# Optimization experiments

Hardware: AMD Instinct MI355X
Metric: run time of the kernel (lower is better)

## Reference

```python
import jax, jax.numpy as jnp
import numpy as np

D_FEAT = 8192   # feature-space dimension d
T_RES = 2048    # number of reservoir feature vectors
P_PARAMS = 16   # n_modes * ansatz_layers
ORDER = 16      # agp_krylov_order (Krylov/Lanczos subspace size)
DTAU = 0.08     # cfg.ite_dtau
REG = 1e-4      # cfg.agp_reg
EPS = 1e-15


def setup_inputs() -> dict:
    key = jax.random.key(0)
    k1, k2, k3 = jax.random.split(key, 3)
    f = jax.random.normal(k1, (D_FEAT,), jnp.float32)
    # scale so spectral radius of H = -R^T R times DTAU is O(1)
    R = jax.random.normal(k2, (T_RES, D_FEAT), jnp.float32) * 0.02
    D = jax.random.normal(k3, (P_PARAMS, D_FEAT), jnp.float32)
    return {"f": f, "R": R, "D": D}


def _forward(f, R, D):
    d = f.shape[0]
    l = ORDER

    def apply_H(v):
        # H v = -sum_t f_t (f_t . v)  == -R^T (R v), matrix-free, memory-bound
        return -jnp.einsum('td,t->d', R, jnp.einsum('td,d->t', R, v))

    # ITE residual F = -(H - E) f, E = <f, Hf> / <f, f>
    Hf = apply_H(f)
    E = jnp.dot(f, Hf) / (jnp.dot(f, f) + EPS)
    F = -(Hf - E * f)
    normF = jnp.linalg.norm(F)

    # Lanczos with full reorthogonalisation; Q has l+1 rows (last is scratch)
    Q0 = jnp.zeros((l + 1, d), f.dtype).at[0].set(F / normF)
    alpha0 = jnp.zeros((l,), f.dtype)
    beta0 = jnp.zeros((l,), f.dtype)

    def step(carry, j):
        Q, alpha, beta = carry
        qj = Q[j]
        w = apply_H(qj)
        a = jnp.dot(qj, w)
        alpha = alpha.at[j].set(a)
        w = w - a * qj
        jm1 = jnp.maximum(j - 1, 0)
        bprev = jnp.where(j > 0, beta[jm1], jnp.array(0.0, f.dtype))
        w = w - bprev * Q[jm1]
        # full reorthogonalisation; rows > j of Q are zero so this projects
        # exactly onto span{q_0..q_j} like the original k-loop
        w = w - jnp.einsum('kd,k->d', Q, jnp.einsum('kd,d->k', Q, w))
        b = jnp.linalg.norm(w)
        beta = beta.at[j].set(b)
        Q = Q.at[j + 1].set(w / jnp.maximum(b, 1e-30))
        return (Q, alpha, beta), None

    (Q, alpha, beta), _ = jax.lax.scan(step, (Q0, alpha0, beta0), jnp.arange(l))
    Qb = Q[:l]          # (l, d) orthonormal Krylov basis
    off = beta[:l - 1]  # off-diagonal of tridiagonal T

    # Krylov exponential: exp(-H dtau) F ~= ||F|| * Q^T expm(-T dtau) e0
    Tmat = jnp.diag(alpha) + jnp.diag(off, 1) + jnp.diag(off, -1)
    evals, V = jnp.linalg.eigh(Tmat)
    coeffs = normF * (V @ (jnp.exp(-evals * DTAU) * V[0]))
    direction = jnp.einsum('l,ld->d', coeffs, Qb)

    # per-parameter diagonal projection: dtheta_i = <df_i, dir>/(||df_i||^2 + reg)
    dtheta = (D @ direction) / (jnp.sum(D * D, axis=1) + REG)
    return dtheta


def reference(f, R, D):
    return _forward(f, R, D)
```

## Files before the change

kernel.cpp:

```cpp
#include <hip/hip_runtime.h>
#include <math.h>

#define D_FEAT 8192
#define NC4    2048
#define T_RES  2048
#define LORD   16

#define NTHR 512
#define NBLK 256
#define RPT  32
#define NOWN 32
#define CH   64
#define NREPA 4
#define NREPB 16

#define G_COEF  0
#define G_FUPA  16
#define G_FREDB (G_FUPA + 17*NREPA*256)
#define G_FCOEF (G_FREDB + 17*NREPB*16)
#define G_FNUM  (G_FCOEF + NREPB*16)
#define G_ZEND  (G_FNUM + NREPA*256)
#define G_URAW  G_ZEND
#define G_UUP   (G_URAW + 17*2048)
#define G_FFP   (G_UUP + 32)
#define G_B2P   (G_FFP + 256)
#define G_DP    (G_B2P + 16*256)
#define G_NUMP  (G_DP + 16*16*32)
#define G_DENP  (G_NUMP + 16*256)
#define G_UPB   ((G_DENP + 16*256 + 1023) & ~1023)
#define UPSLOT  (NOWN*NBLK*CH)

__device__ __forceinline__ void astore(float* p, float v) {
    __hip_atomic_store(p, v, __ATOMIC_RELAXED, __HIP_MEMORY_SCOPE_AGENT);
}
__device__ __forceinline__ void astoreu(unsigned* p, unsigned v) {
    __hip_atomic_store(p, v, __ATOMIC_RELAXED, __HIP_MEMORY_SCOPE_AGENT);
}
__device__ __forceinline__ unsigned aloadu(const unsigned* p) {
    return __hip_atomic_load(p, __ATOMIC_RELAXED, __HIP_MEMORY_SCOPE_AGENT);
}

__device__ __forceinline__ void sigA(unsigned* fl, int bid) {
    __syncthreads();
    if (threadIdx.x < NREPA) astoreu(&fl[threadIdx.x*256 + bid], 1u);
}
__device__ __forceinline__ void pollA(const unsigned* fl, int bid) {
    if (threadIdx.x < 64) {
        const unsigned* p = fl + (bid & (NREPA-1))*256 + 4*threadIdx.x;
        for (;;) {
            unsigned a = aloadu(p) & aloadu(p+1) & aloadu(p+2) & aloadu(p+3);
            if (__all((int)a)) break;
            __builtin_amdgcn_s_sleep(2);
        }
    }
    __syncthreads();
}

__device__ __forceinline__ void sigB(unsigned* fl, int bid) {
    __syncthreads();
    if (threadIdx.x < NREPB)
        __hip_atomic_fetch_or(&fl[threadIdx.x*16], 1u << bid,
                              __ATOMIC_RELAXED, __HIP_MEMORY_SCOPE_AGENT);
}
__device__ __forceinline__ void pollB(const unsigned* fl, int bid) {
    if (threadIdx.x == 0)
        while (aloadu(&fl[(bid & (NREPB-1))*16]) != 0xFFFFFFFFu)
            __builtin_amdgcn_s_sleep(2);
    __syncthreads();
}

__device__ __forceinline__ float wave_sum64(float s) {
    #pragma unroll
    for (int m = 1; m < 64; m <<= 1) s += __shfl_xor(s, m, 64);
    return s;
}
__device__ __forceinline__ float sum32(float s) {
    #pragma unroll
    for (int m = 1; m < 32; m <<= 1) s += __shfl_xor(s, m, 64);
    return s;
}

__device__ __forceinline__ void u_pass_lds(const float4 (&rr)[RPT],
                                           const float* wsl, float* ubuf,
                                           int rg, int cg) {
    const float4 w4 = ((const float4*)wsl)[cg];
    #pragma unroll
    for (int i = 0; i < RPT; ++i) {
        float d = rr[i].x*w4.x + rr[i].y*w4.y + rr[i].z*w4.z + rr[i].w*w4.w;
        d += __shfl_xor(d, 1, 64);
        d += __shfl_xor(d, 2, 64);
        d += __shfl_xor(d, 4, 64);
        if (cg == 0) ubuf[rg + 64*i] = d;
    }
}

__device__ __forceinline__ void flush_up(float* UP, const float* ubuf,
                                         int bid, int tid) {
    #pragma unroll
    for (int r = 0; r < 4; ++r) {
        const int t = tid + 512*r;
        astore(&UP[(size_t)(t >> 6)*(NBLK*CH) + bid*CH + (t & 63)], ubuf[t]);
    }
}

__device__ __forceinline__ void reduce_up64(const float* __restrict__ UP,
                                            float* udst, float (*red8)[CH],
                                            float* ufin64, float* uhrow,
                                            int bid, int tid) {
    const int r = tid & 63, bg = tid >> 6;
    const float* base = UP + (size_t)bid*(NBLK*CH);
    float s = 0.f;
    #pragma unroll
    for (int m = 0; m < 32; ++m) s += base[(bg*32 + m)*CH + r];
    red8[bg][r] = s;
    __syncthreads();
    if (tid < 64) {
        float u = 0.f;
        #pragma unroll
        for (int g = 0; g < 8; ++g) u += red8[g][tid];
        ufin64[tid] = u;
        uhrow[tid] = u;
        astore(&udst[bid*CH + tid], u);
    }
    __syncthreads();
}

__device__ __forceinline__ float4 y_pass(const float4 (&rr)[RPT],
                                         const float* u, int rg) {
    float4 acc = make_float4(0.f, 0.f, 0.f, 0.f);
    #pragma unroll
    for (int i = 0; i < RPT; ++i) {
        const float ut = u[rg + 64*i];
        acc.x -= ut*rr[i].x; acc.y -= ut*rr[i].y;
        acc.z -= ut*rr[i].z; acc.w -= ut*rr[i].w;
    }
    return acc;
}

__device__ __forceinline__ void y_reduce(float4 acc, float (*red)[8][4],
                                         float* ysl, int wave, int lane, int tid) {
    #pragma unroll
    for (int m = 8; m < 64; m <<= 1) {
        acc.x += __shfl_xor(acc.x, m, 64); acc.y += __shfl_xor(acc.y, m, 64);
        acc.z += __shfl_xor(acc.z, m, 64); acc.w += __shfl_xor(acc.w, m, 64);
    }
    if (lane < 8) {
        red[wave][lane][0] = acc.x; red[wave][lane][1] = acc.y;
        red[wave][lane][2] = acc.z; red[wave][lane][3] = acc.w;
    }
    __syncthreads();
    if (tid < 32) {
        const int g = tid >> 2, comp = tid & 3;
        float s = 0.f;
        #pragma unroll
        for (int w = 0; w < 8; ++w) s += red[w][g][comp];
        ysl[g*4 + comp] = s;
    }
    __syncthreads();
}

__global__ __launch_bounds__(NTHR, 2) void k_all(
    const float* __restrict__ Rm, const float* __restrict__ f,
    const float* __restrict__ Dm, float* __restrict__ out,
    float* __restrict__ ws)
{
    __shared__ __align__(16) float ubuf[2048];
    __shared__ float red8[8][CH];
    __shared__ float red[8][8][4];
    __shared__ float ufin64[CH];
    __shared__ float uh[17][CH];
    __shared__ __align__(16) float ysl[32];
    __shared__ __align__(16) float dirs[32];
    __shared__ __align__(16) float fsl[32];
    __shared__ float Wh[LORD][32];
    __shared__ float bh[LORD];
    __shared__ float alph[LORD];
    __shared__ float dotl[LORD];
    __shared__ float cf[LORD];
    __shared__ float misc[4];

    float* coefg    = ws + G_COEF;
    unsigned* fupA  = (unsigned*)(ws + G_FUPA);
    unsigned* fredB = (unsigned*)(ws + G_FREDB);
    unsigned* fcoef = (unsigned*)(ws + G_FCOEF);
    unsigned* fnum  = (unsigned*)(ws + G_FNUM);
    float* uraw = ws + G_URAW;
    float* UUP  = ws + G_UUP;
    float* FFP  = ws + G_FFP;
    float* B2P  = ws + G_B2P;
    float* DP   = ws + G_DP;
    float* NUMP = ws + G_NUMP;
    float* DENP = ws + G_DENP;
    float* UPB  = ws + G_UPB;

    const int tid = threadIdx.x, bid = blockIdx.x;
    const int cg = tid & 7, rg = tid >> 3;
    const int lane = tid & 63, wave = tid >> 6;
    const bool owner = bid < NOWN;

    const float4* R4 = (const float4*)Rm;
    float4 rr[RPT];
    #pragma unroll
    for (int i = 0; i < RPT; ++i)
        rr[i] = R4[(size_t)(rg + 64*i)*NC4 + (bid << 3) + cg];

    if (wave == 0) {
        float4 fv = make_float4(0.f, 0.f, 0.f, 0.f);
        if (lane < 8) { fv = ((const float4*)f)[(bid << 3) + lane];
                        ((float4*)fsl)[lane] = fv; }
        float s2 = fv.x*fv.x + fv.y*fv.y + fv.z*fv.z + fv.w*fv.w;
        s2 += __shfl_xor(s2, 1, 64);
        s2 += __shfl_xor(s2, 2, 64);
        s2 += __shfl_xor(s2, 4, 64);
        if (lane == 0) astore(&FFP[bid], s2);
    }
    __syncthreads();
    u_pass_lds(rr, fsl, ubuf, rg, cg);
    __syncthreads();
    flush_up(UPB + (size_t)16*UPSLOT, ubuf, bid, tid);
    sigA(fupA + 16*NREPA*256, bid);

    if (owner) {
        pollA(fupA + 16*NREPA*256, bid);
        reduce_up64(UPB + (size_t)16*UPSLOT, uraw + 16*2048, red8, ufin64,
                    uh[16], bid, tid);
        if (wave == 0) {
            float p = ufin64[lane]*ufin64[lane];
            p = wave_sum64(p);
            if (lane == 0) astore(&UUP[bid], p);
        }
        sigB(fredB + 16*NREPB*16, bid);
    }
    pollB(fredB + 16*NREPB*16, bid);

    if (wave == 0) {
        float s = (lane < NOWN) ? UUP[lane] : 0.f;
        s = sum32(s);
        if (lane == 0) misc[3] = s;
    }
    if (wave == 1) {
        float s = 0.f;
        #pragma unroll
        for (int i = 0; i < 4; ++i) s += FFP[lane + 64*i];
        s = wave_sum64(s);
        if (lane == 0) misc[2] = s;
    }
    #pragma unroll
    for (int r = 0; r < 4; ++r)
        ubuf[tid + 512*r] = uraw[16*2048 + tid + 512*r];
    __syncthreads();
    {
        float4 acc = y_pass(rr, ubuf, rg);
        y_reduce(acc, red, ysl, wave, lane, tid);
        const float E = -misc[3] / (misc[2] + 1e-15f);
        float v = 0.f;
        if (tid < 32) { v = E*fsl[tid] - ysl[tid]; Wh[0][tid] = v; }
        if (wave == 0) {
            float s = (lane < 32) ? v*v : 0.f;
            s = wave_sum64(s);
            if (lane == 0) astore(&B2P[0*256 + bid], s);
        }
        __syncthreads();
        u_pass_lds(rr, Wh[0], ubuf, rg, cg);
        __syncthreads();
        flush_up(UPB + (size_t)0*UPSLOT, ubuf, bid, tid);
    }
    sigA(fupA + 0*NREPA*256, bid);

    for (int j = 0; j < LORD; ++j) {
        float* UPj = UPB + (size_t)j*UPSLOT;
        float* DPj = DP + j*(16*NOWN);
        if (owner) {
            pollA(fupA + j*NREPA*256, bid);
            reduce_up64(UPj, uraw + (size_t)j*2048, red8, ufin64, uh[j],
                        bid, tid);
            for (int k = wave; k <= j; k += 8) {
                float p = ufin64[lane] * uh[k][lane];
                p = wave_sum64(p);
                if (lane == 0) astore(&DPj[k*NOWN + bid], p);
            }
            sigB(fredB + j*NREPB*16, bid);
        }
        pollB(fredB + j*NREPB*16, bid);

        float tmp[4];
        if (j < LORD - 1) {
            #pragma unroll
            for (int r = 0; r < 4; ++r)
                tmp[r] = uraw[(size_t)j*2048 + tid + 512*r];
        }
        for (int k = wave; k <= j; k += 8) {
            float s = (lane < NOWN) ? DPj[k*NOWN + lane] : 0.f;
            s = sum32(s);
            if (lane == 0) dotl[k] = s;
        }
        if (wave == 1) {
            float s = 0.f;
            #pragma unroll
            for (int i = 0; i < 4; ++i) s += B2P[j*256 + lane + 64*i];
            s = wave_sum64(s);
            if (lane == 0) misc[0] = s;
        }
        __syncthreads();
        const float b2j = misc[0];
        const float bj  = sqrtf(fmaxf(b2j, 1e-60f));
        if (tid == 0) {
            bh[j]   = bj;
            alph[j] = -dotl[j] / fmaxf(b2j, 1e-60f);
        }
        if (j < LORD - 1) {
            const float inv = 1.0f / bj;
            #pragma unroll
            for (int r = 0; r < 4; ++r) ubuf[tid + 512*r] = tmp[r] * inv;
            __syncthreads();
            float4 acc = y_pass(rr, ubuf, rg);
            y_reduce(acc, red, ysl, wave, lane, tid);
            float v = 0.f;
            if (tid < 32) {
                v = ysl[tid];
                for (int k = 0; k <= j; ++k)
                    v += (dotl[k] / (bj * bh[k] * bh[k])) * Wh[k][tid];
                Wh[j+1][tid] = v;
            }
            if (wave == 0) {
                float s = (lane < 32) ? v*v : 0.f;
                s = wave_sum64(s);
                if (lane == 0) astore(&B2P[(j+1)*256 + bid], s);
            }
            __syncthreads();
            u_pass_lds(rr, Wh[j+1], ubuf, rg, cg);
            __syncthreads();
            flush_up(UPB + (size_t)(j+1)*UPSLOT, ubuf, bid, tid);
            sigA(fupA + (j+1)*NREPA*256, bid);
        } else {
            __syncthreads();
            if (bid == 0 && wave == 0) {
                double a = 0.0, bl = 0.0;
                if (lane < LORD)     a  = (double)alph[lane];
                if (lane < LORD - 1) bl = (double)bh[lane + 1];
                double bprev = __shfl_up(bl, 1, 64);
                if (lane == 0) bprev = 0.0;
                if (lane >= LORD) { a = 0.0; bl = 0.0; bprev = 0.0; }
                double v = (lane == 0) ? 1.0 : 0.0;
                double accd = v;
                for (int n = 1; n <= 30; ++n) {
                    double vm = __shfl_up(v, 1, 64);
                    if (lane == 0) vm = 0.0;
                    double vp = __shfl_down(v, 1, 64);
                    if (lane >= LORD - 1) vp = 0.0;
                    const double tv = a*v + bprev*vm + bl*vp;
                    v = tv * (-0.08 / (double)n);
                    accd += v;
                }
                if (lane < LORD)
                    astore(&coefg[lane], (float)accd * bh[0]);
            }
            __syncthreads();
            if (bid == 0 && tid < NREPB) astoreu(&fcoef[tid*16], 1u);
            if (tid == 0)
                while (aloadu(&fcoef[(bid & (NREPB-1))*16]) == 0u)
                    __builtin_amdgcn_s_sleep(2);
            __syncthreads();
        }
    }

    if (wave == 0 && lane < 16) cf[lane] = coefg[lane];
    __syncthreads();
    if (tid < 32) {
        float s = 0.f;
        #pragma unroll
        for (int l = 0; l < LORD; ++l) s += cf[l] * Wh[l][tid] / bh[l];
        dirs[tid] = s;
    }
    __syncthreads();
    if (wave == 0 && lane < 16) {
        const float4* Dp = (const float4*)Dm + (size_t)lane*NC4 + (bid << 3);
        float num = 0.f, den = 0.f;
        #pragma unroll
        for (int g = 0; g < 8; ++g) {
            const float4 dv = Dp[g];
            const float4 dr = ((const float4*)dirs)[g];
            num += dv.x*dr.x + dv.y*dr.y + dv.z*dr.z + dv.w*dr.w;
            den += dv.x*dv.x + dv.y*dv.y + dv.z*dv.z + dv.w*dv.w;
        }
        astore(&NUMP[lane*256 + bid], num);
        astore(&DENP[lane*256 + bid], den);
    }
    sigA(fnum, bid);

    if (bid == 0) {
        pollA(fnum, 0);
        for (int p = wave; p < 16; p += 8) {
            float n = 0.f, d = 0.f;
            #pragma unroll
            for (int i = 0; i < 4; ++i) {
                n += NUMP[p*256 + lane + 64*i];
                d += DENP[p*256 + lane + 64*i];
            }
            n = wave_sum64(n);
            d = wave_sum64(d);
            if (lane == 0) out[p] = n / (d + 1e-4f);
        }
    }
}

extern "C" void kernel_launch(void* const* d_in, const int* in_sizes, int n_in,
                              void* d_out, int out_size, void* d_ws, size_t ws_size,
                              hipStream_t stream)
{
    (void)in_sizes; (void)n_in; (void)out_size; (void)ws_size;
    const float* f  = (const float*)d_in[0];
    const float* Rm = (const float*)d_in[1];
    const float* Dm = (const float*)d_in[2];
    float* outp = (float*)d_out;
    float* ws   = (float*)d_ws;
    hipMemsetAsync(ws, 0, G_ZEND * sizeof(float), stream);
    void* args[] = { (void*)&Rm, (void*)&f, (void*)&Dm, (void*)&outp, (void*)&ws };
    hipLaunchCooperativeKernel((const void*)k_all, dim3(NBLK), dim3(NTHR),
                               args, 0, stream);
}
```

Baseline: 314.1 us.

## Remap register tile to whole rows per thread and widen owner reduction

Each thread now holds 4 full R rows across the block's 32 columns instead of 32 rows by 4 columns. The u-pass dot products therefore finish in registers without shuffles or an LDS staging buffer, and partials are written with 64-bit atomic stores. The cross-block u reduction is split over 64 owner blocks of 32 rows each, which needs a 64-bit bitmask barrier and a new butterfly-style y reduction. The 1/beta scaling moves after the y reduction. This trades LDS traffic and syncs for more shuffle work in the y pass and more owner participation.

New measurement: 535.2 us. +70.4%, slower.

```diff
diff --git a/kernel.cpp b/kernel.cpp
--- a/kernel.cpp
+++ b/kernel.cpp
@@ -8,11 +8,11 @@
 
 #define NTHR 512
 #define NBLK 256
-#define RPT  32
-#define NOWN 32
-#define CH   64
-#define NREPA 4
+#define CH   32
+#define NOWN 64
+#define NREPA 8
 #define NREPB 16
+#define UPSLOT (NBLK*T_RES)
 
 #define G_COEF  0
 #define G_FUPA  16
@@ -22,21 +22,26 @@
 #define G_ZEND  (G_FNUM + NREPA*256)
 #define G_URAW  G_ZEND
 #define G_UUP   (G_URAW + 17*2048)
-#define G_FFP   (G_UUP + 32)
+#define G_FFP   (G_UUP + 64)
 #define G_B2P   (G_FFP + 256)
 #define G_DP    (G_B2P + 16*256)
-#define G_NUMP  (G_DP + 16*16*32)
+#define G_NUMP  (G_DP + 16*16*64)
 #define G_DENP  (G_NUMP + 16*256)
 #define G_UPB   ((G_DENP + 16*256 + 1023) & ~1023)
-#define UPSLOT  (NOWN*NBLK*CH)
 
 __device__ __forceinline__ void astore(float* p, float v) {
     __hip_atomic_store(p, v, __ATOMIC_RELAXED, __HIP_MEMORY_SCOPE_AGENT);
 }
+__device__ __forceinline__ void astore64(unsigned long long* p, unsigned long long v) {
+    __hip_atomic_store(p, v, __ATOMIC_RELAXED, __HIP_MEMORY_SCOPE_AGENT);
+}
 __device__ __forceinline__ void astoreu(unsigned* p, unsigned v) {
     __hip_atomic_store(p, v, __ATOMIC_RELAXED, __HIP_MEMORY_SCOPE_AGENT);
 }
 __device__ __forceinline__ unsigned aloadu(const unsigned* p) {
+    return __hip_atomic_load(p, __ATOMIC_RELAXED, __HIP_MEMORY_SCOPE_AGENT);
+}
+__device__ __forceinline__ unsigned long long aload64(const unsigned long long* p) {
     return __hip_atomic_load(p, __ATOMIC_RELAXED, __HIP_MEMORY_SCOPE_AGENT);
 }
 
@@ -59,12 +64,14 @@
 __device__ __forceinline__ void sigB(unsigned* fl, int bid) {
     __syncthreads();
     if (threadIdx.x < NREPB)
-        __hip_atomic_fetch_or(&fl[threadIdx.x*16], 1u << bid,
-                              __ATOMIC_RELAXED, __HIP_MEMORY_SCOPE_AGENT);
+        __hip_atomic_fetch_or((unsigned long long*)(fl + threadIdx.x*16),
+                              1ULL << bid, __ATOMIC_RELAXED,
+                              __HIP_MEMORY_SCOPE_AGENT);
 }
 __device__ __forceinline__ void pollB(const unsigned* fl, int bid) {
     if (threadIdx.x == 0)
-        while (aloadu(&fl[(bid & (NREPB-1))*16]) != 0xFFFFFFFFu)
+        while (aload64((const unsigned long long*)(fl + (bid & (NREPB-1))*16))
+               != 0xFFFFFFFFFFFFFFFFULL)
             __builtin_amdgcn_s_sleep(2);
     __syncthreads();
 }
@@ -80,73 +87,86 @@
     return s;
 }
 
-__device__ __forceinline__ void u_pass_lds(const float4 (&rr)[RPT],
-                                           const float* wsl, float* ubuf,
-                                           int rg, int cg) {
-    const float4 w4 = ((const float4*)wsl)[cg];
+__device__ __forceinline__ float4 f4add(float4 a, float4 b) {
+    return make_float4(a.x+b.x, a.y+b.y, a.z+b.z, a.w+b.w);
+}
+__device__ __forceinline__ float4 f4shfl_xor(float4 v, int m) {
+    float4 r;
+    r.x = __shfl_xor(v.x, m, 64); r.y = __shfl_xor(v.y, m, 64);
+    r.z = __shfl_xor(v.z, m, 64); r.w = __shfl_xor(v.w, m, 64);
+    return r;
+}
+
+__device__ __forceinline__ void u_pass_row(const float4 (&rr)[4][8],
+                                           const float* wsl, float (&out)[4]) {
+    float4 w4[8];
     #pragma unroll
-    for (int i = 0; i < RPT; ++i) {
-        float d = rr[i].x*w4.x + rr[i].y*w4.y + rr[i].z*w4.z + rr[i].w*w4.w;
-        d += __shfl_xor(d, 1, 64);
-        d += __shfl_xor(d, 2, 64);
-        d += __shfl_xor(d, 4, 64);
-        if (cg == 0) ubuf[rg + 64*i] = d;
-    }
-}
-
-__device__ __forceinline__ void flush_up(float* UP, const float* ubuf,
-                                         int bid, int tid) {
+    for (int c = 0; c < 8; ++c) w4[c] = ((const float4*)wsl)[c];
     #pragma unroll
     for (int r = 0; r < 4; ++r) {
-        const int t = tid + 512*r;
-        astore(&UP[(size_t)(t >> 6)*(NBLK*CH) + bid*CH + (t & 63)], ubuf[t]);
-    }
-}
-
-__device__ __forceinline__ void reduce_up64(const float* __restrict__ UP,
-                                            float* udst, float (*red8)[CH],
-                                            float* ufin64, float* uhrow,
-                                            int bid, int tid) {
-    const int r = tid & 63, bg = tid >> 6;
-    const float* base = UP + (size_t)bid*(NBLK*CH);
-    float s = 0.f;
-    #pragma unroll
-    for (int m = 0; m < 32; ++m) s += base[(bg*32 + m)*CH + r];
-    red8[bg][r] = s;
-    __syncthreads();
-    if (tid < 64) {
-        float u = 0.f;
-        #pragma unroll
-        for (int g = 0; g < 8; ++g) u += red8[g][tid];
-        ufin64[tid] = u;
-        uhrow[tid] = u;
-        astore(&udst[bid*CH + tid], u);
-    }
-    __syncthreads();
-}
-
-__device__ __forceinline__ float4 y_pass(const float4 (&rr)[RPT],
-                                         const float* u, int rg) {
-    float4 acc = make_float4(0.f, 0.f, 0.f, 0.f);
-    #pragma unroll
-    for (int i = 0; i < RPT; ++i) {
-        const float ut = u[rg + 64*i];
-        acc.x -= ut*rr[i].x; acc.y -= ut*rr[i].y;
-        acc.z -= ut*rr[i].z; acc.w -= ut*rr[i].w;
-    }
-    return acc;
-}
-
-__device__ __forceinline__ void y_reduce(float4 acc, float (*red)[8][4],
-                                         float* ysl, int wave, int lane, int tid) {
-    #pragma unroll
-    for (int m = 8; m < 64; m <<= 1) {
-        acc.x += __shfl_xor(acc.x, m, 64); acc.y += __shfl_xor(acc.y, m, 64);
-        acc.z += __shfl_xor(acc.z, m, 64); acc.w += __shfl_xor(acc.w, m, 64);
-    }
+        float d0 = rr[r][0].x*w4[0].x + rr[r][0].y*w4[0].y + rr[r][0].z*w4[0].z + rr[r][0].w*w4[0].w;
+        float d1 = rr[r][1].x*w4[1].x + rr[r][1].y*w4[1].y + rr[r][1].z*w4[1].z + rr[r][1].w*w4[1].w;
+        float d2 = rr[r][2].x*w4[2].x + rr[r][2].y*w4[2].y + rr[r][2].z*w4[2].z + rr[r][2].w*w4[2].w;
+        float d3 = rr[r][3].x*w4[3].x + rr[r][3].y*w4[3].y + rr[r][3].z*w4[3].z + rr[r][3].w*w4[3].w;
+        float d4 = rr[r][4].x*w4[4].x + rr[r][4].y*w4[4].y + rr[r][4].z*w4[4].z + rr[r][4].w*w4[4].w;
+        float d5 = rr[r][5].x*w4[5].x + rr[r][5].y*w4[5].y + rr[r][5].z*w4[5].z + rr[r][5].w*w4[5].w;
+        float d6 = rr[r][6].x*w4[6].x + rr[r][6].y*w4[6].y + rr[r][6].z*w4[6].z + rr[r][6].w*w4[6].w;
+        float d7 = rr[r][7].x*w4[7].x + rr[r][7].y*w4[7].y + rr[r][7].z*w4[7].z + rr[r][7].w*w4[7].w;
+        out[r] = ((d0+d1)+(d2+d3)) + ((d4+d5)+(d6+d7));
+    }
+}
+
+__device__ __forceinline__ void flush4(float* UP, const float (&out)[4],
+                                       int h, int bid) {
+    const int t0 = h << 2;
+    float* dst = &UP[(size_t)(t0 >> 5)*(NBLK*CH) + bid*CH + (t0 & 31)];
+    unsigned long long p0, p1;
+    __builtin_memcpy(&p0, &out[0], 8);
+    __builtin_memcpy(&p1, &out[2], 8);
+    astore64((unsigned long long*)dst, p0);
+    astore64((unsigned long long*)(dst + 2), p1);
+}
+
+__device__ __forceinline__ void y_reduce8(const float4 (&acc)[8],
+                                          float (*red)[8][4], float* ysl,
+                                          int wave, int lane, int tid) {
+    const bool b0 = lane & 1, b1 = lane & 2, b2 = lane & 4;
+    float4 h0_0, h0_1, h0_2, h0_3;
+    {
+        float4 s0 = b0 ? acc[0] : acc[4];
+        float4 s1 = b0 ? acc[1] : acc[5];
+        float4 s2 = b0 ? acc[2] : acc[6];
+        float4 s3 = b0 ? acc[3] : acc[7];
+        float4 r0 = f4shfl_xor(s0, 1), r1 = f4shfl_xor(s1, 1);
+        float4 r2 = f4shfl_xor(s2, 1), r3 = f4shfl_xor(s3, 1);
+        h0_0 = f4add(b0 ? acc[4] : acc[0], r0);
+        h0_1 = f4add(b0 ? acc[5] : acc[1], r1);
+        h0_2 = f4add(b0 ? acc[6] : acc[2], r2);
+        h0_3 = f4add(b0 ? acc[7] : acc[3], r3);
+    }
+    float4 h1_0, h1_1;
+    {
+        float4 s0 = b1 ? h1_0 : h0_2;
+        (void)s0;
+        float4 t0 = b1 ? h0_0 : h0_2;
+        float4 t1 = b1 ? h0_1 : h0_3;
+        float4 r0 = f4shfl_xor(t0, 2), r1 = f4shfl_xor(t1, 2);
+        h1_0 = f4add(b1 ? h0_2 : h0_0, r0);
+        h1_1 = f4add(b1 ? h0_3 : h0_1, r1);
+    }
+    float4 h2;
+    {
+        float4 t0 = b2 ? h1_0 : h1_1;
+        float4 r0 = f4shfl_xor(t0, 4);
+        h2 = f4add(b2 ? h1_1 : h1_0, r0);
+    }
+    h2 = f4add(h2, f4shfl_xor(h2, 8));
+    h2 = f4add(h2, f4shfl_xor(h2, 16));
+    h2 = f4add(h2, f4shfl_xor(h2, 32));
     if (lane < 8) {
-        red[wave][lane][0] = acc.x; red[wave][lane][1] = acc.y;
-        red[wave][lane][2] = acc.z; red[wave][lane][3] = acc.w;
+        const int G = ((lane & 1) << 2) | (lane & 2) | ((lane >> 2) & 1);
+        red[wave][G][0] = h2.x; red[wave][G][1] = h2.y;
+        red[wave][G][2] = h2.z; red[wave][G][3] = h2.w;
     }
     __syncthreads();
     if (tid < 32) {
@@ -164,15 +184,14 @@
     const float* __restrict__ Dm, float* __restrict__ out,
     float* __restrict__ ws)
 {
-    __shared__ __align__(16) float ubuf[2048];
-    __shared__ float red8[8][CH];
     __shared__ float red[8][8][4];
-    __shared__ float ufin64[CH];
-    __shared__ float uh[17][CH];
+    __shared__ float red2[32][17];
+    __shared__ float ufin32[32];
+    __shared__ float uh[17][32];
     __shared__ __align__(16) float ysl[32];
     __shared__ __align__(16) float dirs[32];
     __shared__ __align__(16) float fsl[32];
-    __shared__ float Wh[LORD][32];
+    __shared__ __align__(16) float Wh[LORD][32];
     __shared__ float bh[LORD];
     __shared__ float alph[LORD];
     __shared__ float dotl[LORD];
@@ -194,15 +213,16 @@
     float* UPB  = ws + G_UPB;
 
     const int tid = threadIdx.x, bid = blockIdx.x;
-    const int cg = tid & 7, rg = tid >> 3;
     const int lane = tid & 63, wave = tid >> 6;
     const bool owner = bid < NOWN;
 
     const float4* R4 = (const float4*)Rm;
-    float4 rr[RPT];
+    float4 rr[4][8];
     #pragma unroll
-    for (int i = 0; i < RPT; ++i)
-        rr[i] = R4[(size_t)(rg + 64*i)*NC4 + (bid << 3) + cg];
+    for (int r = 0; r < 4; ++r)
+        #pragma unroll
+        for (int c = 0; c < 8; ++c)
+            rr[r][c] = R4[(size_t)((tid << 2) + r)*NC4 + (bid << 3) + c];
 
     if (wave == 0) {
         float4 fv = make_float4(0.f, 0.f, 0.f, 0.f);
@@ -215,27 +235,44 @@
         if (lane == 0) astore(&FFP[bid], s2);
     }
     __syncthreads();
-    u_pass_lds(rr, fsl, ubuf, rg, cg);
-    __syncthreads();
-    flush_up(UPB + (size_t)16*UPSLOT, ubuf, bid, tid);
+    {
+        float uo[4];
+        u_pass_row(rr, fsl, uo);
+        flush4(UPB + (size_t)16*UPSLOT, uo, tid, bid);
+    }
     sigA(fupA + 16*NREPA*256, bid);
 
     if (owner) {
         pollA(fupA + 16*NREPA*256, bid);
-        reduce_up64(UPB + (size_t)16*UPSLOT, uraw + 16*2048, red8, ufin64,
-                    uh[16], bid, tid);
+        const float* base = UPB + (size_t)16*UPSLOT + (size_t)bid*(NBLK*CH);
+        const int r = tid & 31, q = tid >> 5;
+        float s = 0.f;
+        #pragma unroll
+        for (int i = 0; i < 16; ++i) s += base[(q*16 + i)*CH + r];
+        red2[r][q] = s;
+        __syncthreads();
+        if (tid < 32) {
+            float u = 0.f;
+            #pragma unroll
+            for (int q2 = 0; q2 < 16; ++q2) u += red2[tid][q2];
+            ufin32[tid] = u;
+            uh[16][tid] = u;
+            astore(&uraw[16*2048 + bid*CH + tid], u);
+        }
+        __syncthreads();
         if (wave == 0) {
-            float p = ufin64[lane]*ufin64[lane];
-            p = wave_sum64(p);
+            float p = (lane < 32) ? ufin32[lane]*ufin32[lane] : 0.f;
+            p = sum32(p);
             if (lane == 0) astore(&UUP[bid], p);
         }
         sigB(fredB + 16*NREPB*16, bid);
     }
     pollB(fredB + 16*NREPB*16, bid);
 
+    float4 u4 = ((const float4*)(uraw + 16*2048))[tid];
     if (wave == 0) {
-        float s = (lane < NOWN) ? UUP[lane] : 0.f;
-        s = sum32(s);
+        float s = UUP[lane];
+        s = wave_sum64(s);
         if (lane == 0) misc[3] = s;
     }
     if (wave == 1) {
@@ -245,13 +282,21 @@
         s = wave_sum64(s);
         if (lane == 0) misc[2] = s;
     }
-    #pragma unroll
-    for (int r = 0; r < 4; ++r)
-        ubuf[tid + 512*r] = uraw[16*2048 + tid + 512*r];
-    __syncthreads();
     {
-        float4 acc = y_pass(rr, ubuf, rg);
-        y_reduce(acc, red, ysl, wave, lane, tid);
+        float4 acc[8];
+        #pragma unroll
+        for (int c = 0; c < 8; ++c) acc[c] = make_float4(0.f, 0.f, 0.f, 0.f);
+        const float ua[4] = {u4.x, u4.y, u4.z, u4.w};
+        #pragma unroll
+        for (int r = 0; r < 4; ++r) {
+            const float ut = ua[r];
+            #pragma unroll
+            for (int c = 0; c < 8; ++c) {
+                acc[c].x -= ut*rr[r][c].x; acc[c].y -= ut*rr[r][c].y;
+                acc[c].z -= ut*rr[r][c].z; acc[c].w -= ut*rr[r][c].w;
+            }
+        }
+        y_reduce8(acc, red, ysl, wave, lane, tid);
         const float E = -misc[3] / (misc[2] + 1e-15f);
         float v = 0.f;
         if (tid < 32) { v = E*fsl[tid] - ysl[tid]; Wh[0][tid] = v; }
@@ -261,9 +306,9 @@
             if (lane == 0) astore(&B2P[0*256 + bid], s);
         }
         __syncthreads();
-        u_pass_lds(rr, Wh[0], ubuf, rg, cg);
-        __syncthreads();
-        flush_up(UPB + (size_t)0*UPSLOT, ubuf, bid, tid);
+        float uo[4];
+        u_pass_row(rr, Wh[0], uo);
+        flush4(UPB + (size_t)0*UPSLOT, uo, tid, bid);
     }
     sigA(fupA + 0*NREPA*256, bid);
 
@@ -272,26 +317,37 @@
         float* DPj = DP + j*(16*NOWN);
         if (owner) {
             pollA(fupA + j*NREPA*256, bid);
-            reduce_up64(UPj, uraw + (size_t)j*2048, red8, ufin64, uh[j],
-                        bid, tid);
+            const float* base = UPj + (size_t)bid*(NBLK*CH);
+            const int r = tid & 31, q = tid >> 5;
+            float s = 0.f;
+            #pragma unroll
+            for (int i = 0; i < 16; ++i) s += base[(q*16 + i)*CH + r];
+            red2[r][q] = s;
+            __syncthreads();
+            if (tid < 32) {
+                float u = 0.f;
+                #pragma unroll
+                for (int q2 = 0; q2 < 16; ++q2) u += red2[tid][q2];
+                ufin32[tid] = u;
+                uh[j][tid] = u;
+                astore(&uraw[(size_t)j*2048 + bid*CH + tid], u);
+            }
+            __syncthreads();
             for (int k = wave; k <= j; k += 8) {
-                float p = ufin64[lane] * uh[k][lane];
-                p = wave_sum64(p);
+                float p = (lane < 32) ? ufin32[lane]*uh[k][lane] : 0.f;
+                p = sum32(p);
                 if (lane == 0) astore(&DPj[k*NOWN + bid], p);
             }
             sigB(fredB + j*NREPB*16, bid);
         }
         pollB(fredB + j*NREPB*16, bid);
 
-        float tmp[4];
-        if (j < LORD - 1) {
-            #pragma unroll
-            for (int r = 0; r < 4; ++r)
-                tmp[r] = uraw[(size_t)j*2048 + tid + 512*r];
-        }
+        float4 uj4 = make_float4(0.f, 0.f, 0.f, 0.f);
+        if (j < LORD - 1)
+            uj4 = ((const float4*)(uraw + (size_t)j*2048))[tid];
         for (int k = wave; k <= j; k += 8) {
-            float s = (lane < NOWN) ? DPj[k*NOWN + lane] : 0.f;
-            s = sum32(s);
+            float s = DPj[k*NOWN + lane];
+            s = wave_sum64(s);
             if (lane == 0) dotl[k] = s;
         }
         if (wave == 1) {
@@ -309,15 +365,24 @@
             alph[j] = -dotl[j] / fmaxf(b2j, 1e-60f);
         }
         if (j < LORD - 1) {
+            float4 acc[8];
+            #pragma unroll
+            for (int c = 0; c < 8; ++c) acc[c] = make_float4(0.f, 0.f, 0.f, 0.f);
+            const float ua[4] = {uj4.x, uj4.y, uj4.z, uj4.w};
+            #pragma unroll
+            for (int r = 0; r < 4; ++r) {
+                const float ut = ua[r];
+                #pragma unroll
+                for (int c = 0; c < 8; ++c) {
+                    acc[c].x -= ut*rr[r][c].x; acc[c].y -= ut*rr[r][c].y;
+                    acc[c].z -= ut*rr[r][c].z; acc[c].w -= ut*rr[r][c].w;
+                }
+            }
+            y_reduce8(acc, red, ysl, wave, lane, tid);
             const float inv = 1.0f / bj;
-            #pragma unroll
-            for (int r = 0; r < 4; ++r) ubuf[tid + 512*r] = tmp[r] * inv;
-            __syncthreads();
-            float4 acc = y_pass(rr, ubuf, rg);
-            y_reduce(acc, red, ysl, wave, lane, tid);
             float v = 0.f;
             if (tid < 32) {
-                v = ysl[tid];
+                v = ysl[tid] * inv;
                 for (int k = 0; k <= j; ++k)
                     v += (dotl[k] / (bj * bh[k] * bh[k])) * Wh[k][tid];
                 Wh[j+1][tid] = v;
@@ -328,9 +393,9 @@
                 if (lane == 0) astore(&B2P[(j+1)*256 + bid], s);
             }
             __syncthreads();
-            u_pass_lds(rr, Wh[j+1], ubuf, rg, cg);
-            __syncthreads();
-            flush_up(UPB + (size_t)(j+1)*UPSLOT, ubuf, bid, tid);
+            float uo[4];
+            u_pass_row(rr, Wh[j+1], uo);
+            flush4(UPB + (size_t)(j+1)*UPSLOT, uo, tid, bid);
             sigA(fupA + (j+1)*NREPA*256, bid);
         } else {
             __syncthreads();
```

## Double owner blocks for the reduction and compute Krylov coefficients redundantly per block

Applied to the files above, without the earlier changes.

Raises the number of reducer (owner) blocks from 32 to 64, each reducing a 32-wide chunk instead of 64, which halves the serial reduction work per owner. The phase-B flag changes from a single bitmask fetch_or to per-owner flags polled by a wave. Every block now computes the final Taylor-series coefficients itself, which removes a grid-wide broadcast and wait through global memory. The cost is more flag traffic and polling, plus redundant double-precision work in every block.

Result: faster. 307.2 us (-2.2%).

```diff
diff --git a/kernel.cpp b/kernel.cpp
--- a/kernel.cpp
+++ b/kernel.cpp
@@ -9,23 +9,21 @@
 #define NTHR 512
 #define NBLK 256
 #define RPT  32
-#define NOWN 32
-#define CH   64
-#define NREPA 4
+#define NOWN 64
+#define CH   32
+#define NREPA 8
 #define NREPB 16
 
-#define G_COEF  0
-#define G_FUPA  16
+#define G_FUPA  0
 #define G_FREDB (G_FUPA + 17*NREPA*256)
-#define G_FCOEF (G_FREDB + 17*NREPB*16)
-#define G_FNUM  (G_FCOEF + NREPB*16)
+#define G_FNUM  (G_FREDB + 17*NREPB*NOWN)
 #define G_ZEND  (G_FNUM + NREPA*256)
 #define G_URAW  G_ZEND
 #define G_UUP   (G_URAW + 17*2048)
-#define G_FFP   (G_UUP + 32)
+#define G_FFP   (G_UUP + 64)
 #define G_B2P   (G_FFP + 256)
 #define G_DP    (G_B2P + 16*256)
-#define G_NUMP  (G_DP + 16*16*32)
+#define G_NUMP  (G_DP + 16*16*64)
 #define G_DENP  (G_NUMP + 16*256)
 #define G_UPB   ((G_DENP + 16*256 + 1023) & ~1023)
 #define UPSLOT  (NOWN*NBLK*CH)
@@ -58,14 +56,14 @@
 
 __device__ __forceinline__ void sigB(unsigned* fl, int bid) {
     __syncthreads();
-    if (threadIdx.x < NREPB)
-        __hip_atomic_fetch_or(&fl[threadIdx.x*16], 1u << bid,
-                              __ATOMIC_RELAXED, __HIP_MEMORY_SCOPE_AGENT);
+    if (threadIdx.x < NREPB) astoreu(&fl[threadIdx.x*NOWN + bid], 1u);
 }
 __device__ __forceinline__ void pollB(const unsigned* fl, int bid) {
-    if (threadIdx.x == 0)
-        while (aloadu(&fl[(bid & (NREPB-1))*16]) != 0xFFFFFFFFu)
+    if (threadIdx.x < 64) {
+        const unsigned* p = fl + (bid & (NREPB-1))*NOWN + threadIdx.x;
+        while (!__all(aloadu(p) != 0u))
             __builtin_amdgcn_s_sleep(2);
+    }
     __syncthreads();
 }
 
@@ -99,26 +97,26 @@
     #pragma unroll
     for (int r = 0; r < 4; ++r) {
         const int t = tid + 512*r;
-        astore(&UP[(size_t)(t >> 6)*(NBLK*CH) + bid*CH + (t & 63)], ubuf[t]);
-    }
-}
-
-__device__ __forceinline__ void reduce_up64(const float* __restrict__ UP,
-                                            float* udst, float (*red8)[CH],
-                                            float* ufin64, float* uhrow,
+        astore(&UP[(size_t)(t >> 5)*(NBLK*CH) + bid*CH + (t & 31)], ubuf[t]);
+    }
+}
+
+__device__ __forceinline__ void reduce_up32(const float* __restrict__ UP,
+                                            float* udst, float (*red2)[17],
+                                            float* ufin32, float* uhrow,
                                             int bid, int tid) {
-    const int r = tid & 63, bg = tid >> 6;
+    const int r = tid & 31, q = tid >> 5;
     const float* base = UP + (size_t)bid*(NBLK*CH);
     float s = 0.f;
     #pragma unroll
-    for (int m = 0; m < 32; ++m) s += base[(bg*32 + m)*CH + r];
-    red8[bg][r] = s;
-    __syncthreads();
-    if (tid < 64) {
+    for (int i = 0; i < 16; ++i) s += base[(q*16 + i)*CH + r];
+    red2[r][q] = s;
+    __syncthreads();
+    if (tid < 32) {
         float u = 0.f;
         #pragma unroll
-        for (int g = 0; g < 8; ++g) u += red8[g][tid];
-        ufin64[tid] = u;
+        for (int q2 = 0; q2 < 16; ++q2) u += red2[tid][q2];
+        ufin32[tid] = u;
         uhrow[tid] = u;
         astore(&udst[bid*CH + tid], u);
     }
@@ -165,10 +163,10 @@
     float* __restrict__ ws)
 {
     __shared__ __align__(16) float ubuf[2048];
-    __shared__ float red8[8][CH];
+    __shared__ float red2[32][17];
     __shared__ float red[8][8][4];
-    __shared__ float ufin64[CH];
-    __shared__ float uh[17][CH];
+    __shared__ float ufin32[32];
+    __shared__ float uh[17][32];
     __shared__ __align__(16) float ysl[32];
     __shared__ __align__(16) float dirs[32];
     __shared__ __align__(16) float fsl[32];
@@ -179,10 +177,8 @@
     __shared__ float cf[LORD];
     __shared__ float misc[4];
 
-    float* coefg    = ws + G_COEF;
     unsigned* fupA  = (unsigned*)(ws + G_FUPA);
     unsigned* fredB = (unsigned*)(ws + G_FREDB);
-    unsigned* fcoef = (unsigned*)(ws + G_FCOEF);
     unsigned* fnum  = (unsigned*)(ws + G_FNUM);
     float* uraw = ws + G_URAW;
     float* UUP  = ws + G_UUP;
@@ -222,20 +218,20 @@
 
     if (owner) {
         pollA(fupA + 16*NREPA*256, bid);
-        reduce_up64(UPB + (size_t)16*UPSLOT, uraw + 16*2048, red8, ufin64,
+        reduce_up32(UPB + (size_t)16*UPSLOT, uraw + 16*2048, red2, ufin32,
                     uh[16], bid, tid);
         if (wave == 0) {
-            float p = ufin64[lane]*ufin64[lane];
-            p = wave_sum64(p);
+            float p = (lane < 32) ? ufin32[lane]*ufin32[lane] : 0.f;
+            p = sum32(p);
             if (lane == 0) astore(&UUP[bid], p);
         }
-        sigB(fredB + 16*NREPB*16, bid);
-    }
-    pollB(fredB + 16*NREPB*16, bid);
+        sigB(fredB + 16*NREPB*NOWN, bid);
+    }
+    pollB(fredB + 16*NREPB*NOWN, bid);
 
     if (wave == 0) {
-        float s = (lane < NOWN) ? UUP[lane] : 0.f;
-        s = sum32(s);
+        float s = UUP[lane];
+        s = wave_sum64(s);
         if (lane == 0) misc[3] = s;
     }
     if (wave == 1) {
@@ -272,16 +268,16 @@
         float* DPj = DP + j*(16*NOWN);
         if (owner) {
             pollA(fupA + j*NREPA*256, bid);
-            reduce_up64(UPj, uraw + (size_t)j*2048, red8, ufin64, uh[j],
+            reduce_up32(UPj, uraw + (size_t)j*2048, red2, ufin32, uh[j],
                         bid, tid);
             for (int k = wave; k <= j; k += 8) {
-                float p = ufin64[lane] * uh[k][lane];
-                p = wave_sum64(p);
+                float p = (lane < 32) ? ufin32[lane]*uh[k][lane] : 0.f;
+                p = sum32(p);
                 if (lane == 0) astore(&DPj[k*NOWN + bid], p);
             }
-            sigB(fredB + j*NREPB*16, bid);
-        }
-        pollB(fredB + j*NREPB*16, bid);
+            sigB(fredB + j*NREPB*NOWN, bid);
+        }
+        pollB(fredB + j*NREPB*NOWN, bid);
 
         float tmp[4];
         if (j < LORD - 1) {
@@ -290,8 +286,8 @@
                 tmp[r] = uraw[(size_t)j*2048 + tid + 512*r];
         }
         for (int k = wave; k <= j; k += 8) {
-            float s = (lane < NOWN) ? DPj[k*NOWN + lane] : 0.f;
-            s = sum32(s);
+            float s = DPj[k*NOWN + lane];
+            s = wave_sum64(s);
             if (lane == 0) dotl[k] = s;
         }
         if (wave == 1) {
@@ -334,7 +330,7 @@
             sigA(fupA + (j+1)*NREPA*256, bid);
         } else {
             __syncthreads();
-            if (bid == 0 && wave == 0) {
+            if (wave == 0) {
                 double a = 0.0, bl = 0.0;
                 if (lane < LORD)     a  = (double)alph[lane];
                 if (lane < LORD - 1) bl = (double)bh[lane + 1];
@@ -353,19 +349,12 @@
                     accd += v;
                 }
                 if (lane < LORD)
-                    astore(&coefg[lane], (float)accd * bh[0]);
+                    cf[lane] = (float)accd * bh[0];
             }
             __syncthreads();
-            if (bid == 0 && tid < NREPB) astoreu(&fcoef[tid*16], 1u);
-            if (tid == 0)
-                while (aloadu(&fcoef[(bid & (NREPB-1))*16]) == 0u)
-                    __builtin_amdgcn_s_sleep(2);
-            __syncthreads();
-        }
-    }
-
-    if (wave == 0 && lane < 16) cf[lane] = coefg[lane];
-    __syncthreads();
+        }
+    }
+
     if (tid < 32) {
         float s = 0.f;
         #pragma unroll
```
